# Kernel optimization log

Measured on AMD Instinct MI355X. Metric: run time of the kernel, lower is better.

Reference implementation:

```python
import jax, jax.numpy as jnp
import numpy as np

B, N, C = 4, 2048, 512
H = 8  # num_heads
HD = C // H  # head_dim = 64


def setup_inputs() -> dict:
    key = jax.random.key(0)
    k_x, k_qkv, k_w, k_b = jax.random.split(key, 4)
    x = jax.random.normal(k_x, (B, N, C), dtype=jnp.float32)
    # torch nn.Linear weights are stored as (out_features, in_features)
    w_qkv = jax.random.normal(k_qkv, (3 * C, C), dtype=jnp.float32) * 0.02  # bias=False
    w_proj = jax.random.normal(k_w, (C, C), dtype=jnp.float32) * 0.02
    b_proj = jax.random.normal(k_b, (C,), dtype=jnp.float32) * 0.02
    return {"x": x, "w_qkv": w_qkv, "w_proj": w_proj, "b_proj": b_proj}


def reference(x, w_qkv, w_proj, b_proj):
    b, n, c = x.shape
    scale = HD ** -0.5
    # QKV projection (no bias): (B,N,C) @ (C,3C) -> (B,N,3C)
    qkv = jnp.einsum('bnc,dc->bnd', x, w_qkv)
    qkv = qkv.reshape(b, n, 3, H, HD).transpose(2, 0, 3, 1, 4)  # (3,B,H,N,HD)
    q, k, v = qkv[0], qkv[1], qkv[2]
    # scaled dot-product attention, full N x N scores
    attn = jnp.einsum('bhqd,bhkd->bhqk', q, k) * scale
    attn = jax.nn.softmax(attn, axis=-1)
    out = jnp.einsum('bhqk,bhkd->bhqd', attn, v)  # (B,H,N,HD)
    out = out.transpose(0, 2, 1, 3).reshape(b, n, c)  # (B,N,C)
    # output projection with bias
    return jnp.einsum('bnc,dc->bnd', out, w_proj) + b_proj
```

## Files before the change

kernel.cpp:

```cpp
#include <hip/hip_runtime.h>

typedef _Float16 f16;
typedef _Float16 f16x4 __attribute__((ext_vector_type(4)));
typedef _Float16 f16x8 __attribute__((ext_vector_type(8)));
typedef __fp16 fp16x2 __attribute__((ext_vector_type(2)));
typedef float f32x4 __attribute__((ext_vector_type(4)));

static __device__ __forceinline__ f32x4 mfma_k32(f16x8 a, f16x8 b, f32x4 c) {
  return __builtin_amdgcn_mfma_f32_16x16x32_f16(a, b, c, 0, 0, 0);
}
static __device__ __forceinline__ f32x4 mfma_k16(f16x4 a, f16x4 b, f32x4 c) {
  return __builtin_amdgcn_mfma_f32_16x16x16f16(a, b, c, 0, 0, 0);
}
static __device__ __forceinline__ void gll16(const f16* g, f16* l) {
  __builtin_amdgcn_global_load_lds(
      (const __attribute__((address_space(1))) void*)g,
      (__attribute__((address_space(3))) void*)l, 16, 0, 0);
}

#define BN 2048
#define CC 512
#define NHD 64
#define MROWS 8192
#define SLAB ((size_t)32 * BN * NHD)
#define CH 64
#define EPAD 136
#define QSCALE 0.1803368801111204f

__global__ __launch_bounds__(256)
void cvt_f16(const float* __restrict__ X, const float* __restrict__ Wq,
             const float* __restrict__ Wp, f16* __restrict__ x16,
             f16* __restrict__ wq16, f16* __restrict__ wp16) {
  const int idx = blockIdx.x * 256 + threadIdx.x;
  const int stride = gridDim.x * 256;
  for (int i = idx; i < (MROWS * CC) / 4; i += stride) {
    float4 v = ((const float4*)X)[i];
    f16x4 h = {(f16)v.x, (f16)v.y, (f16)v.z, (f16)v.w};
    ((f16x4*)x16)[i] = h;
  }
  for (int i = idx; i < (3 * CC * CC) / 4; i += stride) {
    float4 v = ((const float4*)Wq)[i];
    f16x4 h = {(f16)v.x, (f16)v.y, (f16)v.z, (f16)v.w};
    ((f16x4*)wq16)[i] = h;
  }
  for (int i = idx; i < (CC * CC) / 4; i += stride) {
    float4 v = ((const float4*)Wp)[i];
    f16x4 h = {(f16)v.x, (f16)v.y, (f16)v.z, (f16)v.w};
    ((f16x4*)wp16)[i] = h;
  }
}

__global__ __launch_bounds__(256)
void qkv_gemm(const f16* __restrict__ X, const f16* __restrict__ W,
              f16* __restrict__ qkv) {
  __shared__ __align__(16) f16 As[128 * 32];
  __shared__ __align__(16) f16 Bs[128 * 32];
  __shared__ __align__(16) f16 ep[64 * EPAD];
  const int t = threadIdx.x;
  const int lane = t & 63, wave = t >> 6;
  const int wr = wave >> 1, wc = wave & 1;
  const int mt = blockIdx.x / 12, nt = blockIdx.x % 12;
  const int m0 = mt * 128, n0 = nt * 128;
  const int grp = lane >> 4, lid = lane & 15;

  const int srow = 32 * wave + (lane >> 2);
  const int gslot = (lane & 3) ^ ((lane >> 2) & 3);
  const int ga0 = (m0 + srow) * CC + gslot * 8;
  const int gb0 = (n0 + srow) * CC + gslot * 8;
  f16* const ldsA = As + wave * 1024;
  f16* const ldsB = Bs + wave * 1024;

  const int abase = wr * 2048 + lid * 32 + (grp ^ (lid & 3)) * 8;
  const int bbase = wc * 2048 + lid * 32 + (grp ^ (lid & 3)) * 8;

  const f32x4 zf = {0.f, 0.f, 0.f, 0.f};
  f32x4 acc[4][4];
#pragma unroll
  for (int i = 0; i < 4; i++)
#pragma unroll
    for (int j = 0; j < 4; j++) acc[i][j] = zf;

  for (int k0 = 0; k0 < CC; k0 += 32) {
    gll16(X + ga0 + k0, ldsA);
    gll16(X + ga0 + 16 * CC + k0, ldsA + 512);
    gll16(W + gb0 + k0, ldsB);
    gll16(W + gb0 + 16 * CC + k0, ldsB + 512);
    __syncthreads();
    f16x8 af[4], bf[4];
#pragma unroll
    for (int mi = 0; mi < 4; mi++)
      af[mi] = *(const f16x8*)&As[abase + mi * 512];
#pragma unroll
    for (int ni = 0; ni < 4; ni++)
      bf[ni] = *(const f16x8*)&Bs[bbase + ni * 512];
#pragma unroll
    for (int mi = 0; mi < 4; mi++)
#pragma unroll
      for (int ni = 0; ni < 4; ni++)
        acc[mi][ni] = mfma_k32(af[mi], bf[ni], acc[mi][ni]);
    __syncthreads();
  }

  const int s = n0 >> 9;
  const int b = m0 >> 11;
  const int nbase = m0 & 2047;
  if (s == 2) {
#pragma unroll
    for (int ph = 0; ph < 2; ++ph) {
      if (wc == ph) {
#pragma unroll
        for (int mi = 0; mi < 4; mi++) {
          int kloc = wr * 64 + mi * 16 + grp * 4;
          int pos = (kloc & ~31) | (grp << 3) | ((mi & 1) << 2);
#pragma unroll
          for (int ni = 0; ni < 4; ni++) {
            f16x4 pk = {(f16)acc[mi][ni][0], (f16)acc[mi][ni][1],
                        (f16)acc[mi][ni][2], (f16)acc[mi][ni][3]};
            *(f16x4*)&ep[(ni * 16 + lid) * EPAD + pos] = pk;
          }
        }
      }
      __syncthreads();
#pragma unroll
      for (int u = 0; u < 4; ++u) {
        int unit = t + u * 256;
        int row = unit >> 4, seg = unit & 15;
        int dg = n0 + ph * 64 + row;
        int h = (dg & 511) >> 6, hd = dg & 63;
        f16x8 v = *(const f16x8*)&ep[row * EPAD + seg * 8];
        *(f16x8*)&qkv[2 * SLAB + ((size_t)((b * 8 + h) * 64 + hd)) * BN +
                      nbase + seg * 8] = v;
      }
      __syncthreads();
    }
  } else {
    const float scale = (s == 0) ? QSCALE : 1.0f;
#pragma unroll
    for (int ph = 0; ph < 2; ++ph) {
      if (wr == ph) {
#pragma unroll
        for (int mi = 0; mi < 4; mi++)
#pragma unroll
          for (int ni = 0; ni < 4; ni++)
#pragma unroll
            for (int i = 0; i < 4; i++)
              ep[(mi * 16 + grp * 4 + i) * EPAD + wc * 64 + ni * 16 + lid] =
                  (f16)(acc[mi][ni][i] * scale);
      }
      __syncthreads();
#pragma unroll
      for (int u = 0; u < 4; ++u) {
        int unit = t + u * 256;
        int row = unit >> 4, seg = unit & 15;
        int row_g = m0 + ph * 64 + row;
        int n = row_g & 2047;
        int d_g = n0 + seg * 8;
        int h = (d_g & 511) >> 6, hd = d_g & 63;
        f16x8 v = *(const f16x8*)&ep[row * EPAD + seg * 8];
        *(f16x8*)&qkv[(size_t)s * SLAB +
                      ((size_t)((b * 8 + h) * BN + n)) * 64 + hd] = v;
      }
      __syncthreads();
    }
  }
}

__global__ __launch_bounds__(256)
void attn(const f16* __restrict__ qkv, f16* __restrict__ O) {
  __shared__ __align__(16) char smem[32768];

  const int bh = blockIdx.x & 31;
  const int qb = blockIdx.x >> 5;
  const f16* Q = qkv + (size_t)bh * BN * NHD;
  const f16* K = qkv + SLAB + (size_t)bh * BN * NHD;
  const f16* VT = qkv + 2 * SLAB + (size_t)bh * (size_t)NHD * BN;
  const int t = threadIdx.x, lane = t & 63, wave = t >> 6;
  const int grp = lane >> 4, qv = lane & 15;
  const int qrow = qb * 64 + wave * 16 + qv;
  const int xr = (qv & 7) << 4;

  char* const kaddr0 = smem + qv * 128 + ((grp * 16) ^ xr);
  char* const kaddr1 = smem + qv * 128 + ((grp * 16 + 64) ^ xr);

  const int srow = wave * 16 + (lane >> 3);
  const int scol = (lane & 7) ^ (lane >> 3);
  const int lo_k0 = srow * NHD + scol * 8;
  const int lo_k1 = (srow + 8) * NHD + scol * 8;
  const int lo_v0 = srow * BN + scol * 8;
  const int lo_v1 = (srow + 8) * BN + scol * 8;
  f16* const dK = (f16*)(smem + wave * 2048);
  f16* const dV = (f16*)(smem + 16384 + wave * 2048);

  f16x8 qf0 = *(const f16x8*)(Q + (size_t)qrow * NHD + grp * 8);
  f16x8 qf1 = *(const f16x8*)(Q + (size_t)qrow * NHD + 32 + grp * 8);

  const f32x4 zf = {0.f, 0.f, 0.f, 0.f};
  const f16x4 ones = {(f16)1.f, (f16)1.f, (f16)1.f, (f16)1.f};
  f32x4 acc[4];
#pragma unroll
  for (int i = 0; i < 4; i++) acc[i] = zf;
  f32x4 lacc = zf;

  int koff = 0, voff = 0;
  gll16(K + lo_k0, dK);
  gll16(K + lo_k1, dK + 512);
  gll16(VT + lo_v0, dV);
  gll16(VT + lo_v1, dV + 512);
  koff = CH * NHD; voff = CH;
  __syncthreads();

#define ATTN_BODY(BUF, PF)                                                    \
  {                                                                           \
    if (PF) {                                                                 \
      gll16(K + koff + lo_k0, dK + (BUF ^ 1) * 4096);                         \
      gll16(K + koff + lo_k1, dK + (BUF ^ 1) * 4096 + 512);                   \
      gll16(VT + voff + lo_v0, dV + (BUF ^ 1) * 4096);                        \
      gll16(VT + voff + lo_v1, dV + (BUF ^ 1) * 4096 + 512);                  \
      koff += CH * NHD; voff += CH;                                           \
    }                                                                         \
    __builtin_amdgcn_s_setprio(1);                                            \
    _Pragma("unroll")                                                         \
    for (int kt2 = 0; kt2 < 2; kt2++) {                                       \
      char* const ka = kt2 ? kaddr1 : kaddr0;                                 \
      f16x8 k0a = *(const f16x8*)(kaddr0 + BUF * 8192 + kt2 * 4096);          \
      f16x8 k1a = *(const f16x8*)(kaddr1 + BUF * 8192 + kt2 * 4096);          \
      f32x4 st0 = mfma_k32(k1a, qf1, mfma_k32(k0a, qf0, zf));                 \
      f16x8 k0b = *(const f16x8*)(kaddr0 + BUF * 8192 + kt2 * 4096 + 2048);   \
      f16x8 k1b = *(const f16x8*)(kaddr1 + BUF * 8192 + kt2 * 4096 + 2048);   \
      f32x4 st1 = mfma_k32(k1b, qf1, mfma_k32(k0b, qf0, zf));                 \
      union { f16x4 v; fp16x2 h[2]; } u0, u1;                                 \
      u0.h[0] = __builtin_amdgcn_cvt_pkrtz(exp2f(st0[0]), exp2f(st0[1]));     \
      u0.h[1] = __builtin_amdgcn_cvt_pkrtz(exp2f(st0[2]), exp2f(st0[3]));     \
      u1.h[0] = __builtin_amdgcn_cvt_pkrtz(exp2f(st1[0]), exp2f(st1[1]));     \
      u1.h[1] = __builtin_amdgcn_cvt_pkrtz(exp2f(st1[2]), exp2f(st1[3]));     \
      f16x4 pb0 = u0.v, pb1 = u1.v;                                           \
      lacc = mfma_k16(ones, pb0, lacc);                                       \
      lacc = mfma_k16(ones, pb1, lacc);                                       \
      _Pragma("unroll")                                                       \
      for (int dt = 0; dt < 4; dt++) {                                        \
        union { f16x8 w; f16x4 h4[2]; } uv;                                   \
        uv.w = *(const f16x8*)(ka + 16384 + BUF * 8192 + dt * 2048);          \
        acc[dt] = mfma_k16(uv.h4[0], pb0, acc[dt]);                           \
        acc[dt] = mfma_k16(uv.h4[1], pb1, acc[dt]);                           \
      }                                                                       \
    }                                                                         \
    __builtin_amdgcn_s_setprio(0);                                            \
    __syncthreads();                                                          \
  }

  for (int p = 0; p < 15; ++p) {
    ATTN_BODY(0, 1)
    ATTN_BODY(1, 1)
  }
  ATTN_BODY(0, 1)
  ATTN_BODY(1, 0)
#undef ATTN_BODY

  const int b = bh >> 3, h = bh & 7;
  float inv = 1.0f / lacc[0];
#pragma unroll
  for (int dt = 0; dt < 4; dt++) {
    f16x4 o = {(f16)(acc[dt][0] * inv), (f16)(acc[dt][1] * inv),
               (f16)(acc[dt][2] * inv), (f16)(acc[dt][3] * inv)};
    *(f16x4*)&O[((size_t)(b * BN + qrow)) * CC + h * NHD + dt * 16 + grp * 4] = o;
  }
}

__global__ __launch_bounds__(256)
void proj_gemm(const f16* __restrict__ A, const f16* __restrict__ W,
               const float* __restrict__ bias, float* __restrict__ out) {
  __shared__ __align__(16) f16 As[64 * 32];
  __shared__ __align__(16) f16 Bs[128 * 32];
  const int t = threadIdx.x;
  const int lane = t & 63, wave = t >> 6;
  const int wr = wave >> 1, wc = wave & 1;
  const int mt = blockIdx.x >> 2, nt = blockIdx.x & 3;
  const int m0 = mt * 64, n0 = nt * 128;
  const int grp = lane >> 4, lid = lane & 15;

  const int gslot = (lane & 3) ^ ((lane >> 2) & 3);
  const int ga0 = (m0 + wave * 16 + (lane >> 2)) * CC + gslot * 8;
  const int gb0 = (n0 + wave * 32 + (lane >> 2)) * CC + gslot * 8;
  f16* const ldsA = As + wave * 512;
  f16* const ldsB = Bs + wave * 1024;
  const int abase = (wr * 32 + lid) * 32 + (grp ^ (lid & 3)) * 8;
  const int bbase = (wc * 64 + lid) * 32 + (grp ^ (lid & 3)) * 8;

  const f32x4 zf = {0.f, 0.f, 0.f, 0.f};
  f32x4 acc[2][4];
#pragma unroll
  for (int i = 0; i < 2; i++)
#pragma unroll
    for (int j = 0; j < 4; j++) acc[i][j] = zf;

  for (int k0 = 0; k0 < CC; k0 += 32) {
    gll16(A + ga0 + k0, ldsA);
    gll16(W + gb0 + k0, ldsB);
    gll16(W + gb0 + 16 * CC + k0, ldsB + 512);
    __syncthreads();
    f16x8 af[2], bf[4];
#pragma unroll
    for (int mi = 0; mi < 2; mi++)
      af[mi] = *(const f16x8*)&As[abase + mi * 512];
#pragma unroll
    for (int ni = 0; ni < 4; ni++)
      bf[ni] = *(const f16x8*)&Bs[bbase + ni * 512];
#pragma unroll
    for (int mi = 0; mi < 2; mi++)
#pragma unroll
      for (int ni = 0; ni < 4; ni++)
        acc[mi][ni] = mfma_k32(af[mi], bf[ni], acc[mi][ni]);
    __syncthreads();
  }
#pragma unroll
  for (int mi = 0; mi < 2; mi++) {
#pragma unroll
    for (int ni = 0; ni < 4; ni++) {
      int d = n0 + wc * 64 + ni * 16 + lid;
      float bv = bias[d];
#pragma unroll
      for (int i = 0; i < 4; i++) {
        int row = m0 + wr * 32 + mi * 16 + grp * 4 + i;
        out[(size_t)row * CC + d] = acc[mi][ni][i] + bv;
      }
    }
  }
}

extern "C" void kernel_launch(void* const* d_in, const int* in_sizes, int n_in,
                              void* d_out, int out_size, void* d_ws, size_t ws_size,
                              hipStream_t stream) {
  const float* x = (const float*)d_in[0];
  const float* w_qkv = (const float*)d_in[1];
  const float* w_proj = (const float*)d_in[2];
  const float* b_proj = (const float*)d_in[3];
  float* out = (float*)d_out;

  f16* qkv = (f16*)d_ws;
  f16* Obuf = qkv + 3 * SLAB;
  f16* x16 = Obuf;
  f16* wq16 = Obuf + (size_t)MROWS * CC;
  f16* wp16 = wq16 + (size_t)3 * CC * CC;

  cvt_f16<<<dim3(1024), dim3(256), 0, stream>>>(x, w_qkv, w_proj, x16, wq16, wp16);
  qkv_gemm<<<dim3(64 * 12), dim3(256), 0, stream>>>(x16, wq16, qkv);
  attn<<<dim3(32 * 32), dim3(256), 0, stream>>>(qkv, Obuf);
  proj_gemm<<<dim3(128 * 4), dim3(256), 0, stream>>>(Obuf, wp16, b_proj, out);
}
```

Before: 104.9 us.

## Double-buffer GEMM LDS loads and merge attention MFMAs into K32 form

The QKV and projection GEMMs now use two LDS buffers. The next k-slice is prefetched while the current one is multiplied, which removes one barrier per iteration. In attention, the paired 16x16x16 MFMAs for the row-sum and P·V are merged into single 16x16x32 MFMAs over concatenated operands, halving the instruction count. The cost is doubled LDS use in the GEMMs, which may lower occupancy.

```diff
diff --git a/kernel.cpp b/kernel.cpp
--- a/kernel.cpp
+++ b/kernel.cpp
@@ -8,9 +8,6 @@
 
 static __device__ __forceinline__ f32x4 mfma_k32(f16x8 a, f16x8 b, f32x4 c) {
   return __builtin_amdgcn_mfma_f32_16x16x32_f16(a, b, c, 0, 0, 0);
-}
-static __device__ __forceinline__ f32x4 mfma_k16(f16x4 a, f16x4 b, f32x4 c) {
-  return __builtin_amdgcn_mfma_f32_16x16x16f16(a, b, c, 0, 0, 0);
 }
 static __device__ __forceinline__ void gll16(const f16* g, f16* l) {
   __builtin_amdgcn_global_load_lds(
@@ -53,8 +50,8 @@
 __global__ __launch_bounds__(256)
 void qkv_gemm(const f16* __restrict__ X, const f16* __restrict__ W,
               f16* __restrict__ qkv) {
-  __shared__ __align__(16) f16 As[128 * 32];
-  __shared__ __align__(16) f16 Bs[128 * 32];
+  __shared__ __align__(16) f16 As[2 * 4096];
+  __shared__ __align__(16) f16 Bs[2 * 4096];
   __shared__ __align__(16) f16 ep[64 * EPAD];
   const int t = threadIdx.x;
   const int lane = t & 63, wave = t >> 6;
@@ -67,8 +64,6 @@
   const int gslot = (lane & 3) ^ ((lane >> 2) & 3);
   const int ga0 = (m0 + srow) * CC + gslot * 8;
   const int gb0 = (n0 + srow) * CC + gslot * 8;
-  f16* const ldsA = As + wave * 1024;
-  f16* const ldsB = Bs + wave * 1024;
 
   const int abase = wr * 2048 + lid * 32 + (grp ^ (lid & 3)) * 8;
   const int bbase = wc * 2048 + lid * 32 + (grp ^ (lid & 3)) * 8;
@@ -80,26 +75,44 @@
 #pragma unroll
     for (int j = 0; j < 4; j++) acc[i][j] = zf;
 
-  for (int k0 = 0; k0 < CC; k0 += 32) {
-    gll16(X + ga0 + k0, ldsA);
-    gll16(X + ga0 + 16 * CC + k0, ldsA + 512);
-    gll16(W + gb0 + k0, ldsB);
-    gll16(W + gb0 + 16 * CC + k0, ldsB + 512);
-    __syncthreads();
-    f16x8 af[4], bf[4];
-#pragma unroll
-    for (int mi = 0; mi < 4; mi++)
-      af[mi] = *(const f16x8*)&As[abase + mi * 512];
-#pragma unroll
-    for (int ni = 0; ni < 4; ni++)
-      bf[ni] = *(const f16x8*)&Bs[bbase + ni * 512];
-#pragma unroll
-    for (int mi = 0; mi < 4; mi++)
-#pragma unroll
-      for (int ni = 0; ni < 4; ni++)
-        acc[mi][ni] = mfma_k32(af[mi], bf[ni], acc[mi][ni]);
-    __syncthreads();
-  }
+  gll16(X + ga0, As + wave * 1024);
+  gll16(X + ga0 + 16 * CC, As + wave * 1024 + 512);
+  gll16(W + gb0, Bs + wave * 1024);
+  gll16(W + gb0 + 16 * CC, Bs + wave * 1024 + 512);
+  __syncthreads();
+
+#define QKV_STEP(BUF, NEXTK, PF)                                              \
+  {                                                                           \
+    if (PF) {                                                                 \
+      gll16(X + ga0 + (NEXTK), As + (BUF ^ 1) * 4096 + wave * 1024);          \
+      gll16(X + ga0 + 16 * CC + (NEXTK),                                      \
+            As + (BUF ^ 1) * 4096 + wave * 1024 + 512);                       \
+      gll16(W + gb0 + (NEXTK), Bs + (BUF ^ 1) * 4096 + wave * 1024);          \
+      gll16(W + gb0 + 16 * CC + (NEXTK),                                      \
+            Bs + (BUF ^ 1) * 4096 + wave * 1024 + 512);                       \
+    }                                                                         \
+    f16x8 af[4], bf[4];                                                       \
+    _Pragma("unroll")                                                         \
+    for (int mi = 0; mi < 4; mi++)                                            \
+      af[mi] = *(const f16x8*)&As[(BUF) * 4096 + abase + mi * 512];           \
+    _Pragma("unroll")                                                         \
+    for (int ni = 0; ni < 4; ni++)                                            \
+      bf[ni] = *(const f16x8*)&Bs[(BUF) * 4096 + bbase + ni * 512];           \
+    _Pragma("unroll")                                                         \
+    for (int mi = 0; mi < 4; mi++)                                            \
+      _Pragma("unroll")                                                       \
+      for (int ni = 0; ni < 4; ni++)                                          \
+        acc[mi][ni] = mfma_k32(af[mi], bf[ni], acc[mi][ni]);                  \
+    __syncthreads();                                                          \
+  }
+
+  for (int p = 0; p < 7; ++p) {
+    QKV_STEP(0, 64 * p + 32, 1)
+    QKV_STEP(1, 64 * p + 64, 1)
+  }
+  QKV_STEP(0, 480, 1)
+  QKV_STEP(1, 0, 0)
+#undef QKV_STEP
 
   const int s = n0 >> 9;
   const int b = m0 >> 11;
@@ -195,7 +208,8 @@
   f16x8 qf1 = *(const f16x8*)(Q + (size_t)qrow * NHD + 32 + grp * 8);
 
   const f32x4 zf = {0.f, 0.f, 0.f, 0.f};
-  const f16x4 ones = {(f16)1.f, (f16)1.f, (f16)1.f, (f16)1.f};
+  const f16x8 ones8 = {(f16)1.f, (f16)1.f, (f16)1.f, (f16)1.f,
+                       (f16)1.f, (f16)1.f, (f16)1.f, (f16)1.f};
   f32x4 acc[4];
 #pragma unroll
   for (int i = 0; i < 4; i++) acc[i] = zf;
@@ -228,20 +242,17 @@
       f16x8 k0b = *(const f16x8*)(kaddr0 + BUF * 8192 + kt2 * 4096 + 2048);   \
       f16x8 k1b = *(const f16x8*)(kaddr1 + BUF * 8192 + kt2 * 4096 + 2048);   \
       f32x4 st1 = mfma_k32(k1b, qf1, mfma_k32(k0b, qf0, zf));                 \
-      union { f16x4 v; fp16x2 h[2]; } u0, u1;                                 \
-      u0.h[0] = __builtin_amdgcn_cvt_pkrtz(exp2f(st0[0]), exp2f(st0[1]));     \
-      u0.h[1] = __builtin_amdgcn_cvt_pkrtz(exp2f(st0[2]), exp2f(st0[3]));     \
-      u1.h[0] = __builtin_amdgcn_cvt_pkrtz(exp2f(st1[0]), exp2f(st1[1]));     \
-      u1.h[1] = __builtin_amdgcn_cvt_pkrtz(exp2f(st1[2]), exp2f(st1[3]));     \
-      f16x4 pb0 = u0.v, pb1 = u1.v;                                           \
-      lacc = mfma_k16(ones, pb0, lacc);                                       \
-      lacc = mfma_k16(ones, pb1, lacc);                                       \
+      union { f16x8 w; fp16x2 h[4]; } up;                                     \
+      up.h[0] = __builtin_amdgcn_cvt_pkrtz(exp2f(st0[0]), exp2f(st0[1]));     \
+      up.h[1] = __builtin_amdgcn_cvt_pkrtz(exp2f(st0[2]), exp2f(st0[3]));     \
+      up.h[2] = __builtin_amdgcn_cvt_pkrtz(exp2f(st1[0]), exp2f(st1[1]));     \
+      up.h[3] = __builtin_amdgcn_cvt_pkrtz(exp2f(st1[2]), exp2f(st1[3]));     \
+      f16x8 p8 = up.w;                                                        \
+      lacc = mfma_k32(ones8, p8, lacc);                                       \
       _Pragma("unroll")                                                       \
       for (int dt = 0; dt < 4; dt++) {                                        \
-        union { f16x8 w; f16x4 h4[2]; } uv;                                   \
-        uv.w = *(const f16x8*)(ka + 16384 + BUF * 8192 + dt * 2048);          \
-        acc[dt] = mfma_k16(uv.h4[0], pb0, acc[dt]);                           \
-        acc[dt] = mfma_k16(uv.h4[1], pb1, acc[dt]);                           \
+        f16x8 v8 = *(const f16x8*)(ka + 16384 + BUF * 8192 + dt * 2048);      \
+        acc[dt] = mfma_k32(v8, p8, acc[dt]);                                  \
       }                                                                       \
     }                                                                         \
     __builtin_amdgcn_s_setprio(0);                                            \
@@ -269,8 +280,8 @@
 __global__ __launch_bounds__(256)
 void proj_gemm(const f16* __restrict__ A, const f16* __restrict__ W,
                const float* __restrict__ bias, float* __restrict__ out) {
-  __shared__ __align__(16) f16 As[64 * 32];
-  __shared__ __align__(16) f16 Bs[128 * 32];
+  __shared__ __align__(16) f16 As[2 * 2048];
+  __shared__ __align__(16) f16 Bs[2 * 4096];
   const int t = threadIdx.x;
   const int lane = t & 63, wave = t >> 6;
   const int wr = wave >> 1, wc = wave & 1;
@@ -281,8 +292,6 @@
   const int gslot = (lane & 3) ^ ((lane >> 2) & 3);
   const int ga0 = (m0 + wave * 16 + (lane >> 2)) * CC + gslot * 8;
   const int gb0 = (n0 + wave * 32 + (lane >> 2)) * CC + gslot * 8;
-  f16* const ldsA = As + wave * 512;
-  f16* const ldsB = Bs + wave * 1024;
   const int abase = (wr * 32 + lid) * 32 + (grp ^ (lid & 3)) * 8;
   const int bbase = (wc * 64 + lid) * 32 + (grp ^ (lid & 3)) * 8;
 
@@ -293,25 +302,42 @@
 #pragma unroll
     for (int j = 0; j < 4; j++) acc[i][j] = zf;
 
-  for (int k0 = 0; k0 < CC; k0 += 32) {
-    gll16(A + ga0 + k0, ldsA);
-    gll16(W + gb0 + k0, ldsB);
-    gll16(W + gb0 + 16 * CC + k0, ldsB + 512);
-    __syncthreads();
-    f16x8 af[2], bf[4];
-#pragma unroll
-    for (int mi = 0; mi < 2; mi++)
-      af[mi] = *(const f16x8*)&As[abase + mi * 512];
-#pragma unroll
-    for (int ni = 0; ni < 4; ni++)
-      bf[ni] = *(const f16x8*)&Bs[bbase + ni * 512];
-#pragma unroll
-    for (int mi = 0; mi < 2; mi++)
-#pragma unroll
-      for (int ni = 0; ni < 4; ni++)
-        acc[mi][ni] = mfma_k32(af[mi], bf[ni], acc[mi][ni]);
-    __syncthreads();
-  }
+  gll16(A + ga0, As + wave * 512);
+  gll16(W + gb0, Bs + wave * 1024);
+  gll16(W + gb0 + 16 * CC, Bs + wave * 1024 + 512);
+  __syncthreads();
+
+#define PROJ_STEP(BUF, NEXTK, PF)                                             \
+  {                                                                           \
+    if (PF) {                                                                 \
+      gll16(A + ga0 + (NEXTK), As + (BUF ^ 1) * 2048 + wave * 512);           \
+      gll16(W + gb0 + (NEXTK), Bs + (BUF ^ 1) * 4096 + wave * 1024);          \
+      gll16(W + gb0 + 16 * CC + (NEXTK),                                      \
+            Bs + (BUF ^ 1) * 4096 + wave * 1024 + 512);                       \
+    }                                                                         \
+    f16x8 af[2], bf[4];                                                       \
+    _Pragma("unroll")                                                         \
+    for (int mi = 0; mi < 2; mi++)                                            \
+      af[mi] = *(const f16x8*)&As[(BUF) * 2048 + abase + mi * 512];           \
+    _Pragma("unroll")                                                         \
+    for (int ni = 0; ni < 4; ni++)                                            \
+      bf[ni] = *(const f16x8*)&Bs[(BUF) * 4096 + bbase + ni * 512];           \
+    _Pragma("unroll")                                                         \
+    for (int mi = 0; mi < 2; mi++)                                            \
+      _Pragma("unroll")                                                       \
+      for (int ni = 0; ni < 4; ni++)                                          \
+        acc[mi][ni] = mfma_k32(af[mi], bf[ni], acc[mi][ni]);                  \
+    __syncthreads();                                                          \
+  }
+
+  for (int p = 0; p < 7; ++p) {
+    PROJ_STEP(0, 64 * p + 32, 1)
+    PROJ_STEP(1, 64 * p + 64, 1)
+  }
+  PROJ_STEP(0, 480, 1)
+  PROJ_STEP(1, 0, 0)
+#undef PROJ_STEP
+
 #pragma unroll
   for (int mi = 0; mi < 2; mi++) {
 #pragma unroll
```

Result: slower. 112.7 us (+7.4%).
